# Optimization experiments

Measured on AMD Instinct MI355X. Metric: run time of the kernel, lower is better.

## Reference

```python
import jax, jax.numpy as jnp
import numpy as np

CHEBYSHEV_K = 5  # number of Chebyshev polynomial terms


def setup_inputs() -> dict:
    key = jax.random.key(0)
    k1, k2, k3 = jax.random.split(key, 3)
    B, N, F_in, F_out = 1024, 512, 16, 8
    x = jax.random.normal(k1, (B, N, F_in), dtype=jnp.float32)
    # symmetric scaled-Laplacian-like matrix, scaled small so recurrence stays stable
    A = jax.random.normal(k2, (N, N), dtype=jnp.float32) / jnp.sqrt(jnp.float32(N))
    L = 0.5 * (A + A.T)
    # xavier-uniform-like weights [K, F_in, F_out]
    limit = np.sqrt(6.0 / (F_in + F_out)).astype(np.float32)
    W = jax.random.uniform(k3, (CHEBYSHEV_K, F_in, F_out), dtype=jnp.float32,
                           minval=-limit, maxval=limit)
    b = jnp.zeros((F_out,), dtype=jnp.float32)
    return {"x": x, "L": L, "W": W, "b": b}


def reference(x, L, W, b):
    # x: [B, N, F_in], L: [N, N], W: [K, F_in, F_out], b: [F_out]
    Lx = lambda z: jnp.einsum('nm,bmf->bnf', L, z)
    Z0 = x
    Z1 = Lx(x)
    out = Z0 @ W[0] + Z1 @ W[1]
    for k in range(2, CHEBYSHEV_K):  # small fixed K, structural loop
        Zk = 2.0 * Lx(Z1) - Z0
        out = out + Zk @ W[k]
        Z0, Z1 = Z1, Zk
    return out + b
```

## Files before the change

### kernel.cpp

```cpp
#include <hip/hip_runtime.h>
#include <cstdint>
#include <cstddef>


typedef __attribute__((ext_vector_type(8))) short  frag_ab;
typedef __attribute__((ext_vector_type(4))) float  frag_cd;

constexpr int BN  = 512;
constexpr int FIN = 16;
constexpr int FOUT= 8;
constexpr int GK  = 5 * BN;
constexpr int PG  = 64;
constexpr int LDST= BN + 8;
constexpr int ZBUF= 64 * LDST;

__device__ __forceinline__ uint16_t f2bf(float f) {
    uint32_t u = __builtin_bit_cast(uint32_t, f);
    u += 0x7FFFu + ((u >> 16) & 1u);
    return (uint16_t)(u >> 16);
}
__device__ __forceinline__ float bf2f(uint16_t h) {
    uint32_t u = ((uint32_t)h) << 16;
    return __builtin_bit_cast(float, u);
}

__device__ __forceinline__ size_t pfrag(int mt, int g, int lane) {
    return ((size_t)(mt * PG + g) * 64 + lane) * 8;
}
__device__ __forceinline__ size_t pelem(int k, int row, int col) {
    return pfrag(row >> 4, (k - 1) * 16 + (col >> 5),
                 ((col >> 3) & 3) * 16 + (row & 15)) + (col & 7);
}
__device__ __forceinline__ size_t lfrag16(int mt, int kt, int lane) {
    return ((size_t)(mt * 16 + kt) * 64 + lane) * 8;
}
__device__ __forceinline__ size_t aswz(int row, int k) {
    return lfrag16(row >> 4, k >> 5, ((k >> 3) & 3) * 16 + (row & 15)) + (k & 7);
}
__device__ __forceinline__ size_t yfrag(int jt16, int g, int lane) {
    return ((size_t)(jt16 * 80 + g) * 64 + lane) * 8;
}

__global__ __launch_bounds__(256)
void prep(const float* __restrict__ x, const float* __restrict__ Lf,
          const float* __restrict__ W, uint16_t* __restrict__ Pcat,
          uint16_t* __restrict__ Llo, uint16_t* __restrict__ Yf) {
    int bid = blockIdx.x, tid = threadIdx.x;
    if (bid < 2048) {
        int t = bid * 256 + tid;
        int jlow = t & 15;
        int moct = (t >> 4) & 63;
        int jhi  = t >> 10;
        int b  = jhi * 2 + (jlow >> 3);
        int fo = jlow & 7;
        int m0 = moct * 8;
        float wr[5][16];
#pragma unroll
        for (int k = 0; k < 5; ++k)
#pragma unroll
            for (int f = 0; f < 16; ++f)
                wr[k][f] = W[(k * 16 + f) * 8 + fo];
        float tmp[5][8];
        const float* xb = x + (size_t)b * (BN * FIN) + (size_t)m0 * FIN;
#pragma unroll
        for (int r = 0; r < 8; ++r) {
            float xr[16];
#pragma unroll
            for (int fi = 0; fi < 4; ++fi) {
                float4 u = *reinterpret_cast<const float4*>(xb + r * FIN + fi * 4);
                xr[fi * 4 + 0] = u.x; xr[fi * 4 + 1] = u.y;
                xr[fi * 4 + 2] = u.z; xr[fi * 4 + 3] = u.w;
            }
#pragma unroll
            for (int k = 0; k < 5; ++k) {
                float s = 0.f;
#pragma unroll
                for (int f = 0; f < 16; ++f) s += xr[f] * wr[k][f];
                tmp[k][r] = s;
            }
        }
#pragma unroll
        for (int k = 0; k < 5; ++k) {
            frag_ab o;
#pragma unroll
            for (int j = 0; j < 8; ++j) o[j] = (short)f2bf(tmp[k][j]);
            *reinterpret_cast<frag_ab*>(
                Yf + yfrag(jhi, k * 16 + (moct >> 2), (moct & 3) * 16 + jlow)) = o;
        }
    } else {
        int t = (bid - 2048) * 256 + tid;
        int lane = t & 63, f = t >> 6;
        int mt = f >> 4, kt = f & 15;
        int row = mt * 16 + (lane & 15);
        int k0  = kt * 32 + (lane >> 4) * 8;
        const float4* p = reinterpret_cast<const float4*>(Lf + (size_t)row * BN + k0);
        float4 u0 = p[0], u1 = p[1];
        float v[8] = {u0.x, u0.y, u0.z, u0.w, u1.x, u1.y, u1.z, u1.w};
        frag_ab hi, lo;
#pragma unroll
        for (int j = 0; j < 8; ++j) {
            uint16_t h = f2bf(v[j]);
            hi[j] = (short)h;
            lo[j] = (short)f2bf(v[j] - bf2f(h));
        }
        *reinterpret_cast<frag_ab*>(Pcat + pfrag(mt, kt, lane)) = hi;
        *reinterpret_cast<frag_ab*>(Llo + lfrag16(mt, kt, lane)) = lo;
    }
}

__global__ __launch_bounds__(512)
void p2k(uint16_t* __restrict__ Pcat, const uint16_t* __restrict__ Llo,
         uint16_t* __restrict__ P2lo) {
    int tid = threadIdx.x, wv = tid >> 6, lane = tid & 63;
    int lr = lane & 15, q = lane >> 4;
    int id = blockIdx.x * 8 + wv;
    int to = id >> 5, jt = id & 31;
    frag_cd acc = {0.f, 0.f, 0.f, 0.f};
#pragma unroll
    for (int ks = 0; ks < 16; ++ks) {
        frag_ab ahi = *reinterpret_cast<const frag_ab*>(Pcat + pfrag(to, ks, lane));
        frag_ab alo = *reinterpret_cast<const frag_ab*>(Llo + lfrag16(to, ks, lane));
        frag_ab bhi = *reinterpret_cast<const frag_ab*>(Pcat + pfrag(jt, ks, lane));
        frag_ab blo = *reinterpret_cast<const frag_ab*>(Llo + lfrag16(jt, ks, lane));
        acc = __builtin_amdgcn_mfma_f32_16x16x32_bf16(ahi, bhi, acc, 0, 0, 0);
        acc = __builtin_amdgcn_mfma_f32_16x16x32_bf16(alo, bhi, acc, 0, 0, 0);
        acc = __builtin_amdgcn_mfma_f32_16x16x32_bf16(ahi, blo, acc, 0, 0, 0);
    }
#pragma unroll
    for (int r = 0; r < 4; ++r) {
        int row = to * 16 + q * 4 + r, col = jt * 16 + lr;
        float v = 2.f * acc[r] - ((row == col) ? 1.f : 0.f);
        uint16_t h = f2bf(v);
        Pcat[pelem(2, row, col)] = h;
        P2lo[aswz(row, col)] = f2bf(v - bf2f(h));
    }
}

__global__ __launch_bounds__(512)
void p34k(uint16_t* __restrict__ Pcat, const uint16_t* __restrict__ Llo,
          const uint16_t* __restrict__ P2lo) {
    int tid = threadIdx.x, wv = tid >> 6, lane = tid & 63;
    int lr = lane & 15, q = lane >> 4;
    int id = blockIdx.x * 8 + wv;
    bool isP3 = id < 1024;
    int id2 = isP3 ? id : id - 1024;
    int to = id2 >> 5, jt = id2 & 31;
    int agoff = isP3 ? 0 : 16;
    const uint16_t* aLo = isP3 ? Llo : P2lo;
    frag_cd acc = {0.f, 0.f, 0.f, 0.f};
#pragma unroll
    for (int ks = 0; ks < 16; ++ks) {
        frag_ab ahi = *reinterpret_cast<const frag_ab*>(Pcat + pfrag(to, agoff + ks, lane));
        frag_ab alo = *reinterpret_cast<const frag_ab*>(aLo + lfrag16(to, ks, lane));
        frag_ab bhi = *reinterpret_cast<const frag_ab*>(Pcat + pfrag(jt, 16 + ks, lane));
        frag_ab blo = *reinterpret_cast<const frag_ab*>(P2lo + lfrag16(jt, ks, lane));
        acc = __builtin_amdgcn_mfma_f32_16x16x32_bf16(ahi, bhi, acc, 0, 0, 0);
        acc = __builtin_amdgcn_mfma_f32_16x16x32_bf16(alo, bhi, acc, 0, 0, 0);
        acc = __builtin_amdgcn_mfma_f32_16x16x32_bf16(ahi, blo, acc, 0, 0, 0);
    }
#pragma unroll
    for (int r = 0; r < 4; ++r) {
        int row = to * 16 + q * 4 + r, col = jt * 16 + lr;
        if (isP3) {
            float sub = bf2f(Pcat[pelem(1, row, col)]) + bf2f(Llo[aswz(row, col)]);
            Pcat[pelem(3, row, col)] = f2bf(2.f * acc[r] - sub);
        } else {
            float sub = (row == col) ? 1.f : 0.f;
            Pcat[pelem(4, row, col)] = f2bf(2.f * acc[r] - sub);
        }
    }
}

__global__ __launch_bounds__(512)
void chebgemm(const uint16_t* __restrict__ Pcat, const uint16_t* __restrict__ Yf,
              const float* __restrict__ bvec, float* __restrict__ out) {
    __shared__ float fbuf[16384];
    int bid = blockIdx.x;
    int xcd = bid & 7, n = bid >> 3;
    int jt  = xcd * 8 + (n >> 2);
    int mtB = n & 3;
    int tid = threadIdx.x, wv = tid >> 6, lane = tid & 63;
    int lr = lane & 15, q = lane >> 4;
    int wm = wv >> 2, wj = wv & 3;

    frag_cd acc[4][2] = {};
#pragma unroll 2
    for (int kt = 0; kt < 64; ++kt) {
        frag_ab aF[4], bF[2];
#pragma unroll
        for (int mi = 0; mi < 4; ++mi)
            aF[mi] = *reinterpret_cast<const frag_ab*>(
                Pcat + pfrag(mtB * 8 + wm * 4 + mi, kt, lane));
#pragma unroll
        for (int cj = 0; cj < 2; ++cj)
            bF[cj] = *reinterpret_cast<const frag_ab*>(
                Yf + yfrag(jt * 8 + wj * 2 + cj, 16 + kt, lane));
#pragma unroll
        for (int mi = 0; mi < 4; ++mi)
#pragma unroll
            for (int cj = 0; cj < 2; ++cj)
                acc[mi][cj] = __builtin_amdgcn_mfma_f32_16x16x32_bf16(
                    aF[mi], bF[cj], acc[mi][cj], 0, 0, 0);
    }
#pragma unroll
    for (int mi = 0; mi < 4; ++mi)
#pragma unroll
        for (int cj = 0; cj < 2; ++cj) {
            int jt16 = jt * 8 + wj * 2 + cj;
#pragma unroll
            for (int r = 0; r < 4; ++r) {
                int nloc = wm * 64 + mi * 16 + q * 4 + r;
                int ng = mtB * 128 + nloc;
                float y0 = bf2f(Yf[yfrag(jt16, ng >> 5, ((ng >> 3) & 3) * 16 + lr)
                                   + (ng & 7)]);
                fbuf[nloc * 128 + wj * 32 + cj * 16 + lr] = acc[mi][cj][r] + y0;
            }
        }
    __syncthreads();
    float4 bv0 = *reinterpret_cast<const float4*>(bvec);
    float4 bv1 = *(reinterpret_cast<const float4*>(bvec) + 1);
#pragma unroll
    for (int i = 0; i < 8; ++i) {
        int idx = i * 2048 + tid * 4;
        int bb = idx >> 10, r = idx & 1023, nn = r >> 3, fo = r & 7;
        float4 v = *reinterpret_cast<const float4*>(fbuf + nn * 128 + bb * 8 + fo);
        float4 bias = (fo & 4) ? bv1 : bv0;
        v.x += bias.x; v.y += bias.y; v.z += bias.z; v.w += bias.w;
        *reinterpret_cast<float4*>(out + (size_t)(jt * 16 + bb) * 4096
                                       + (size_t)(mtB * 128 + nn) * 8 + fo) = v;
    }
}


__global__ __launch_bounds__(256)
void cvtL_swz(const float* __restrict__ Lf, uint16_t* __restrict__ Lb) {
    int t = blockIdx.x * 256 + threadIdx.x;
    int f = t >> 6, lane = t & 63;
    int mt = f >> 4, ks = f & 15;
    int row = mt * 16 + (lane & 15);
    int k0  = ks * 32 + (lane >> 4) * 8;
    const float4* p = reinterpret_cast<const float4*>(Lf + (size_t)row * BN + k0);
    float4 u0 = p[0], u1 = p[1];
    frag_ab o;
    o[0] = (short)f2bf(u0.x); o[1] = (short)f2bf(u0.y);
    o[2] = (short)f2bf(u0.z); o[3] = (short)f2bf(u0.w);
    o[4] = (short)f2bf(u1.x); o[5] = (short)f2bf(u1.y);
    o[6] = (short)f2bf(u1.z); o[7] = (short)f2bf(u1.w);
    *reinterpret_cast<frag_ab*>(Lb + (size_t)t * 8) = o;
}

__global__ __launch_bounds__(256)
void m2comp(const float* __restrict__ Lf, uint16_t* __restrict__ Mb) {
    const int tid = threadIdx.x;
    const int wv = tid >> 6, lane = tid & 63, lr = lane & 15, q = lane >> 4;
    const int i0 = (blockIdx.x >> 4) * 32 + (wv >> 1) * 16;
    const int j0 = (blockIdx.x & 15) * 32 + (wv & 1) * 16;
    frag_cd acc = {0.f, 0.f, 0.f, 0.f};
    const float* arow = Lf + (size_t)(i0 + lr) * BN;
    const float* brow = Lf + (size_t)(j0 + lr) * BN;
    for (int ks = 0; ks < 16; ++ks) {
        const int kb = ks * 32 + q * 8;
        const float4* ap = reinterpret_cast<const float4*>(arow + kb);
        const float4* bp = reinterpret_cast<const float4*>(brow + kb);
        float4 A0 = ap[0], A1 = ap[1], B0 = bp[0], B1 = bp[1];
        float av[8] = {A0.x, A0.y, A0.z, A0.w, A1.x, A1.y, A1.z, A1.w};
        float bw[8] = {B0.x, B0.y, B0.z, B0.w, B1.x, B1.y, B1.z, B1.w};
        frag_ab ah, al, bh, bl;
#pragma unroll
        for (int j = 0; j < 8; ++j) {
            uint16_t h = f2bf(av[j]);
            ah[j] = (short)h; al[j] = (short)f2bf(av[j] - bf2f(h));
            uint16_t g = f2bf(bw[j]);
            bh[j] = (short)g; bl[j] = (short)f2bf(bw[j] - bf2f(g));
        }
        acc = __builtin_amdgcn_mfma_f32_16x16x32_bf16(ah, bh, acc, 0, 0, 0);
        acc = __builtin_amdgcn_mfma_f32_16x16x32_bf16(ah, bl, acc, 0, 0, 0);
        acc = __builtin_amdgcn_mfma_f32_16x16x32_bf16(al, bh, acc, 0, 0, 0);
    }
#pragma unroll
    for (int r = 0; r < 4; ++r) {
        int i = i0 + q * 4 + r, j = j0 + lr;
        float v = 2.f * acc[r] - ((i == j) ? 1.f : 0.f);
        Mb[aswz(i, j)] = f2bf(v);
    }
}

__global__ __launch_bounds__(512, 2)
void cheb2_kernel(const float* __restrict__ x, const uint16_t* __restrict__ Lb,
                  const uint16_t* __restrict__ Mb, const float* __restrict__ W,
                  const float* __restrict__ bvec, float* __restrict__ out) {
    __shared__ uint16_t ldsb[2 * ZBUF];
    uint16_t* z0 = ldsb;
    uint16_t* z1 = ldsb + ZBUF;
    const int tid = threadIdx.x, wave = tid >> 6, lane = tid & 63;
    const int lr = lane & 15, q = lane >> 4;

    const float4* x4 = reinterpret_cast<const float4*>(x + (size_t)blockIdx.x * (4 * BN * FIN));
    for (int s = 0; s < 2; ++s) {
        int a = tid + s * 512;
        int f0g = a & 3, n8 = (a >> 2) & 63, bl = a >> 8;
        int jb = bl * 2048 + n8 * 32 + f0g;
        float4 v[8];
#pragma unroll
        for (int r = 0; r < 8; ++r) v[r] = x4[jb + r * 4];
        int cb = bl * 16 + f0g * 4, nb = n8 * 8;
#pragma unroll
        for (int w = 0; w < 4; ++w) {
            frag_ab pk;
#pragma unroll
            for (int r = 0; r < 8; ++r)
                pk[r] = (short)f2bf(reinterpret_cast<const float*>(&v[r])[w]);
            *reinterpret_cast<frag_ab*>(&z0[(cb + w) * LDST + nb]) = pk;
        }
    }
    frag_ab wf[3];
#pragma unroll
    for (int p = 0; p < 3; ++p) {
        frag_ab t;
#pragma unroll
        for (int jj = 0; jj < 8; ++jj) {
            int k = q * 8 + jj, ki = p * 2 + (k >> 4), fin = k & 15;
            float val = 0.0f;
            if (lr < 8) {
                int idx = fin * FOUT + lr;
                if      (ki == 0) val = W[idx] - W[4 * 128 + idx];
                else if (ki == 1) val = W[128 + idx] - W[3 * 128 + idx];
                else if (ki < 5)  val = W[ki * 128 + idx];
            }
            t[jj] = (short)f2bf(val);
        }
        wf[p] = t;
    }
    const float bv = (lr < 8) ? bvec[lr] : 0.0f;
    frag_cd accOut[4][4] = {};
    frag_cd acc1[4][4], acc2[4][4];

    auto round = [&](const uint16_t* cur) {
#pragma unroll
        for (int mi = 0; mi < 4; ++mi)
#pragma unroll
            for (int ct = 0; ct < 4; ++ct) {
                acc1[mi][ct] = (frag_cd){0.f, 0.f, 0.f, 0.f};
                acc2[mi][ct] = (frag_cd){0.f, 0.f, 0.f, 0.f};
            }
        for (int ks = 0; ks < 16; ++ks) {
            frag_ab bfr[4];
#pragma unroll
            for (int ct = 0; ct < 4; ++ct)
                bfr[ct] = *reinterpret_cast<const frag_ab*>(
                    cur + (ct * 16 + lr) * LDST + ks * 32 + q * 8);
#pragma unroll
            for (int mi = 0; mi < 4; ++mi) {
                frag_ab a = *reinterpret_cast<const frag_ab*>(
                    Lb + lfrag16(wave + mi * 8, ks, lane));
                frag_ab m = *reinterpret_cast<const frag_ab*>(
                    Mb + lfrag16(wave + mi * 8, ks, lane));
#pragma unroll
                for (int ct = 0; ct < 4; ++ct)
                    acc1[mi][ct] = __builtin_amdgcn_mfma_f32_16x16x32_bf16(
                        a, bfr[ct], acc1[mi][ct], 0, 0, 0);
#pragma unroll
                for (int ct = 0; ct < 4; ++ct)
                    acc2[mi][ct] = __builtin_amdgcn_mfma_f32_16x16x32_bf16(
                        m, bfr[ct], acc2[mi][ct], 0, 0, 0);
            }
        }
    };
    auto wb = [&](frag_cd (&acc)[4][4], uint16_t* dst, float scale) {
#pragma unroll
        for (int mi = 0; mi < 4; ++mi) {
            int row0 = (wave + mi * 8) * 16 + q * 4;
#pragma unroll
            for (int ct = 0; ct < 4; ++ct) {
                uint16_t* dp = dst + (ct * 16 + lr) * LDST + row0;
                ushort4 nv;
                nv.x = f2bf(scale * acc[mi][ct][0]); nv.y = f2bf(scale * acc[mi][ct][1]);
                nv.z = f2bf(scale * acc[mi][ct][2]); nv.w = f2bf(scale * acc[mi][ct][3]);
                *reinterpret_cast<ushort4*>(dp) = nv;
            }
        }
    };
    auto epi = [&](const uint16_t* bA, const uint16_t* bB, frag_ab wfr) {
        const uint16_t* base = (q < 2) ? bA : bB;
        int finb = (q & 1) * 8;
#pragma unroll
        for (int mi = 0; mi < 4; ++mi) {
            int n = (wave + mi * 8) * 16 + lr;
#pragma unroll
            for (int bt = 0; bt < 4; ++bt) {
                const uint16_t* pp = base + (bt * 16 + finb) * LDST + n;
                frag_ab afr;
#pragma unroll
                for (int jj = 0; jj < 8; ++jj) afr[jj] = (short)pp[jj * LDST];
                accOut[mi][bt] = __builtin_amdgcn_mfma_f32_16x16x32_bf16(
                    afr, wfr, accOut[mi][bt], 0, 0, 0);
            }
        }
    };

    __syncthreads();
    round(z0);
    wb(acc1, z1, 1.f);
    __syncthreads();
    epi(z0, z1, wf[0]);
    __syncthreads();
    wb(acc2, z0, 1.f);
    __syncthreads();
    round(z0);
    wb(acc1, z1, 2.f);
    __syncthreads();
    epi(z0, z1, wf[1]);
    __syncthreads();
    wb(acc2, z0, 2.f);
    __syncthreads();
    epi(z0, z0, wf[2]);

    float* fbuf = reinterpret_cast<float*>(z1);
    if (lr < 8) {
#pragma unroll
        for (int mi = 0; mi < 4; ++mi) {
            int n0 = (wave + mi * 8) * 16 + q * 4;
#pragma unroll
            for (int bt = 0; bt < 4; ++bt)
#pragma unroll
                for (int r = 0; r < 4; ++r)
                    fbuf[(bt * BN + n0 + r) * FOUT + lr] = accOut[mi][bt][r] + bv;
        }
    }
    __syncthreads();
    {
        const float4* fb4 = reinterpret_cast<const float4*>(fbuf);
        float4* o4 = reinterpret_cast<float4*>(out + (size_t)blockIdx.x * (4 * BN * FOUT));
#pragma unroll
        for (int i = 0; i < 8; ++i)
            o4[i * 512 + tid] = fb4[i * 512 + tid];
    }
}

__global__ __launch_bounds__(512, 2)
void cheb1_kernel(const float* __restrict__ x, const float* __restrict__ Lf,
                  const float* __restrict__ W, const float* __restrict__ bvec,
                  float* __restrict__ out) {
    __shared__ uint16_t ldsb[2 * ZBUF];
    uint16_t* z0 = ldsb;
    uint16_t* z1 = ldsb + ZBUF;
    const int tid = threadIdx.x, wave = tid >> 6, lane = tid & 63;
    const int lr = lane & 15, q = lane >> 4;
    const float4* x4 = reinterpret_cast<const float4*>(x + (size_t)blockIdx.x * (4 * BN * FIN));
    for (int s = 0; s < 2; ++s) {
        int a = tid + s * 512;
        int f0g = a & 3, n8 = (a >> 2) & 63, bl = a >> 8;
        int jb = bl * 2048 + n8 * 32 + f0g;
        float4 v[8];
#pragma unroll
        for (int r = 0; r < 8; ++r) v[r] = x4[jb + r * 4];
        int cb = bl * 16 + f0g * 4, nb = n8 * 8;
#pragma unroll
        for (int w = 0; w < 4; ++w) {
            frag_ab pk;
#pragma unroll
            for (int r = 0; r < 8; ++r)
                pk[r] = (short)f2bf(reinterpret_cast<const float*>(&v[r])[w]);
            *reinterpret_cast<frag_ab*>(&z0[(cb + w) * LDST + nb]) = pk;
        }
    }
    frag_ab wf[3];
#pragma unroll
    for (int p = 0; p < 3; ++p) {
        frag_ab t;
#pragma unroll
        for (int jj = 0; jj < 8; ++jj) {
            int k = q * 8 + jj, ki = p * 2 + (k >> 4), fin = k & 15;
            float val = (lr < 8 && ki < 5) ? W[ki * 128 + fin * FOUT + lr] : 0.0f;
            t[jj] = (short)f2bf(val);
        }
        wf[p] = t;
    }
    const float bv = (lr < 8) ? bvec[lr] : 0.0f;
    frag_cd accOut[4][4] = {};
    auto loadA = [&](int mt, int ks) -> frag_ab {
        const float4* p = reinterpret_cast<const float4*>(Lf + (size_t)(mt * 16 + lr) * BN + ks * 32 + q * 8);
        float4 u0 = p[0], u1 = p[1];
        frag_ab t;
        t[0] = (short)f2bf(u0.x); t[1] = (short)f2bf(u0.y);
        t[2] = (short)f2bf(u0.z); t[3] = (short)f2bf(u0.w);
        t[4] = (short)f2bf(u1.x); t[5] = (short)f2bf(u1.y);
        t[6] = (short)f2bf(u1.z); t[7] = (short)f2bf(u1.w);
        return t;
    };
    auto app = [&](const uint16_t* cur, uint16_t* dst, bool first) {
        frag_cd acc[4][4] = {};
        for (int ks = 0; ks < 16; ++ks) {
            frag_ab bfr[4];
#pragma unroll
            for (int ct = 0; ct < 4; ++ct)
                bfr[ct] = *reinterpret_cast<const frag_ab*>(
                    cur + (ct * 16 + lr) * LDST + ks * 32 + q * 8);
#pragma unroll
            for (int mi = 0; mi < 4; ++mi) {
                frag_ab a = loadA(wave + mi * 8, ks);
#pragma unroll
                for (int ct = 0; ct < 4; ++ct)
                    acc[mi][ct] = __builtin_amdgcn_mfma_f32_16x16x32_bf16(
                        a, bfr[ct], acc[mi][ct], 0, 0, 0);
            }
        }
#pragma unroll
        for (int mi = 0; mi < 4; ++mi) {
            int row0 = (wave + mi * 8) * 16 + q * 4;
#pragma unroll
            for (int ct = 0; ct < 4; ++ct) {
                uint16_t* dp = dst + (ct * 16 + lr) * LDST + row0;
                float pz[4] = {0.f, 0.f, 0.f, 0.f};
                if (!first) {
                    ushort4 pv = *reinterpret_cast<const ushort4*>(dp);
                    pz[0] = bf2f(pv.x); pz[1] = bf2f(pv.y);
                    pz[2] = bf2f(pv.z); pz[3] = bf2f(pv.w);
                }
                ushort4 nv;
                float v0 = acc[mi][ct][0], v1 = acc[mi][ct][1];
                float v2 = acc[mi][ct][2], v3 = acc[mi][ct][3];
                if (!first) { v0 = 2.f*v0-pz[0]; v1 = 2.f*v1-pz[1];
                              v2 = 2.f*v2-pz[2]; v3 = 2.f*v3-pz[3]; }
                nv.x = f2bf(v0); nv.y = f2bf(v1); nv.z = f2bf(v2); nv.w = f2bf(v3);
                *reinterpret_cast<ushort4*>(dp) = nv;
            }
        }
    };
    auto epi = [&](const uint16_t* bA, const uint16_t* bB, frag_ab wfr) {
        const uint16_t* base = (q < 2) ? bA : bB;
        int finb = (q & 1) * 8;
#pragma unroll
        for (int mi = 0; mi < 4; ++mi) {
            int n = (wave + mi * 8) * 16 + lr;
#pragma unroll
            for (int bt = 0; bt < 4; ++bt) {
                const uint16_t* pp = base + (bt * 16 + finb) * LDST + n;
                frag_ab afr;
#pragma unroll
                for (int jj = 0; jj < 8; ++jj) afr[jj] = (short)pp[jj * LDST];
                accOut[mi][bt] = __builtin_amdgcn_mfma_f32_16x16x32_bf16(
                    afr, wfr, accOut[mi][bt], 0, 0, 0);
            }
        }
    };
    __syncthreads();
    app(z0, z1, true);  __syncthreads();
    epi(z0, z1, wf[0]); __syncthreads();
    app(z1, z0, false); __syncthreads();
    app(z0, z1, false); __syncthreads();
    epi(z0, z1, wf[1]); __syncthreads();
    app(z1, z0, false); __syncthreads();
    epi(z0, z0, wf[2]);
    if (lr < 8) {
        float* ob = out + (size_t)blockIdx.x * 4 * BN * FOUT;
#pragma unroll
        for (int mi = 0; mi < 4; ++mi) {
            int row0 = (wave + mi * 8) * 16 + q * 4;
#pragma unroll
            for (int bt = 0; bt < 4; ++bt) {
                float* op = ob + bt * (BN * FOUT) + row0 * FOUT + lr;
                op[0] = accOut[mi][bt][0] + bv; op[FOUT] = accOut[mi][bt][1] + bv;
                op[2 * FOUT] = accOut[mi][bt][2] + bv; op[3 * FOUT] = accOut[mi][bt][3] + bv;
            }
        }
    }
}

extern "C" void kernel_launch(void* const* d_in, const int* in_sizes, int n_in,
                              void* d_out, int out_size, void* d_ws, size_t ws_size,
                              hipStream_t stream) {
    const float* x  = (const float*)d_in[0];
    const float* Lf = (const float*)d_in[1];
    const float* W  = (const float*)d_in[2];
    const float* bv = (const float*)d_in[3];
    float* out = (float*)d_out;

    const size_t PCAT_B = (size_t)32 * PG * 64 * 8 * 2;
    const size_t LLO_B  = (size_t)BN * BN * 2;
    const size_t P2LO_B = LLO_B;
    const size_t YF_B   = (size_t)512 * 80 * 64 * 8 * 2;
    const size_t matB   = (size_t)BN * BN * 2;

    if (ws_size >= PCAT_B + LLO_B + P2LO_B + YF_B) {
        uint16_t* Pcat = (uint16_t*)d_ws;
        uint16_t* Llo  = Pcat + PCAT_B / 2;
        uint16_t* P2lo = Pcat + (PCAT_B + LLO_B) / 2;
        uint16_t* Yf   = Pcat + (PCAT_B + LLO_B + P2LO_B) / 2;
        prep    <<<dim3(2176), dim3(256), 0, stream>>>(x, Lf, W, Pcat, Llo, Yf);
        p2k     <<<dim3(128),  dim3(512), 0, stream>>>(Pcat, Llo, P2lo);
        p34k    <<<dim3(256),  dim3(512), 0, stream>>>(Pcat, Llo, P2lo);
        chebgemm<<<dim3(256),  dim3(512), 0, stream>>>(Pcat, Yf, bv, out);
    } else if (ws_size >= 2 * matB) {
        uint16_t* Lb = (uint16_t*)d_ws;
        uint16_t* Mb = Lb + (size_t)BN * BN;
        cvtL_swz<<<dim3(128), dim3(256), 0, stream>>>(Lf, Lb);
        m2comp  <<<dim3(256), dim3(256), 0, stream>>>(Lf, Mb);
        cheb2_kernel<<<dim3(256), dim3(512), 0, stream>>>(x, Lb, Mb, W, bv, out);
    } else {
        cheb1_kernel<<<dim3(256), dim3(512), 0, stream>>>(x, Lf, W, bv, out);
    }
}
```

Before: 150.9 us.

## Fuse prep, P2, P3/P4 and Chebyshev GEMM into one cooperative kernel

Replaces the four-kernel sequence (prep, p2k, p34k, chebgemm) with a single cooperative megakernel that uses grid.sync() between phases, with a fallback to the old launches if the cooperative launch fails. The goal is to remove three kernel launch gaps and their tail effects. The fused kernel runs only 256 blocks of 512 threads, so the x@W precompute and Laplacian conversion phases get less parallelism than the old 2176-block prep launch. It also removes the cheb2 fallback path.

```diff
diff --git a/kernel.cpp b/kernel.cpp
--- a/kernel.cpp
+++ b/kernel.cpp
@@ -1,6 +1,9 @@
 #include <hip/hip_runtime.h>
+#include <hip/hip_cooperative_groups.h>
 #include <cstdint>
 #include <cstddef>
+
+namespace cg = cooperative_groups;
 
 
 typedef __attribute__((ext_vector_type(8))) short  frag_ab;
@@ -9,7 +12,6 @@
 constexpr int BN  = 512;
 constexpr int FIN = 16;
 constexpr int FOUT= 8;
-constexpr int GK  = 5 * BN;
 constexpr int PG  = 64;
 constexpr int LDST= BN + 8;
 constexpr int ZBUF= 64 * LDST;
@@ -40,6 +42,201 @@
 __device__ __forceinline__ size_t yfrag(int jt16, int g, int lane) {
     return ((size_t)(jt16 * 80 + g) * 64 + lane) * 8;
 }
+
+__global__ __launch_bounds__(512, 2)
+void megak(const float* __restrict__ x, const float* __restrict__ Lf,
+           const float* __restrict__ W, uint16_t* __restrict__ Pcat,
+           uint16_t* __restrict__ Llo, uint16_t* __restrict__ P2lo,
+           uint16_t* __restrict__ Yf, const float* __restrict__ bvec,
+           float* __restrict__ out) {
+    __shared__ float fbuf[16384];
+    cg::grid_group grid = cg::this_grid();
+    const int tid  = threadIdx.x;
+    const int gtid = blockIdx.x * 512 + tid;
+
+    {
+        int task = gtid >> 1, half = gtid & 1;
+        int b    = task >> 6;
+        int moct = task & 63;
+        int jhi  = b >> 1;
+        int jl0  = (b & 1) * 8;
+        const float* xb = x + (size_t)b * (BN * FIN)
+                            + (size_t)(moct * 8 + half * 4) * FIN;
+        float xr[4][16];
+#pragma unroll
+        for (int r = 0; r < 4; ++r)
+#pragma unroll
+            for (int fi = 0; fi < 4; ++fi) {
+                float4 u = *reinterpret_cast<const float4*>(xb + (size_t)r * FIN + fi * 4);
+                xr[r][fi * 4 + 0] = u.x; xr[r][fi * 4 + 1] = u.y;
+                xr[r][fi * 4 + 2] = u.z; xr[r][fi * 4 + 3] = u.w;
+            }
+#pragma unroll
+        for (int k = 0; k < 5; ++k) {
+            float a[8][4] = {};
+#pragma unroll
+            for (int f = 0; f < 16; ++f) {
+                float x0 = xr[0][f], x1 = xr[1][f], x2 = xr[2][f], x3 = xr[3][f];
+#pragma unroll
+                for (int fo = 0; fo < 8; ++fo) {
+                    float w = W[(k * 16 + f) * 8 + fo];
+                    a[fo][0] += x0 * w; a[fo][1] += x1 * w;
+                    a[fo][2] += x2 * w; a[fo][3] += x3 * w;
+                }
+            }
+#pragma unroll
+            for (int fo = 0; fo < 8; ++fo) {
+                ushort4 o;
+                o.x = f2bf(a[fo][0]); o.y = f2bf(a[fo][1]);
+                o.z = f2bf(a[fo][2]); o.w = f2bf(a[fo][3]);
+                *reinterpret_cast<ushort4*>(
+                    Yf + yfrag(jhi, k * 16 + (moct >> 2), (moct & 3) * 16 + jl0 + fo)
+                       + half * 4) = o;
+            }
+        }
+    }
+    if (gtid < 32768) {
+        int t = gtid;
+        int lane = t & 63, f = t >> 6;
+        int mt = f >> 4, kt = f & 15;
+        int row = mt * 16 + (lane & 15);
+        int k0  = kt * 32 + (lane >> 4) * 8;
+        const float4* p = reinterpret_cast<const float4*>(Lf + (size_t)row * BN + k0);
+        float4 u0 = p[0], u1 = p[1];
+        float v[8] = {u0.x, u0.y, u0.z, u0.w, u1.x, u1.y, u1.z, u1.w};
+        frag_ab hi, lo;
+#pragma unroll
+        for (int j = 0; j < 8; ++j) {
+            uint16_t h = f2bf(v[j]);
+            hi[j] = (short)h;
+            lo[j] = (short)f2bf(v[j] - bf2f(h));
+        }
+        *reinterpret_cast<frag_ab*>(Pcat + pfrag(mt, kt, lane)) = hi;
+        *reinterpret_cast<frag_ab*>(Llo + lfrag16(mt, kt, lane)) = lo;
+    }
+    grid.sync();
+
+    {
+        int wv = tid >> 6, lane = tid & 63;
+        int lr = lane & 15, q = lane >> 4;
+        if (blockIdx.x < 128) {
+            int id = blockIdx.x * 8 + wv;
+            int to = id >> 5, jt = id & 31;
+            frag_cd acc = {0.f, 0.f, 0.f, 0.f};
+#pragma unroll
+            for (int ks = 0; ks < 16; ++ks) {
+                frag_ab ahi = *reinterpret_cast<const frag_ab*>(Pcat + pfrag(to, ks, lane));
+                frag_ab alo = *reinterpret_cast<const frag_ab*>(Llo + lfrag16(to, ks, lane));
+                frag_ab bhi = *reinterpret_cast<const frag_ab*>(Pcat + pfrag(jt, ks, lane));
+                frag_ab blo = *reinterpret_cast<const frag_ab*>(Llo + lfrag16(jt, ks, lane));
+                acc = __builtin_amdgcn_mfma_f32_16x16x32_bf16(ahi, bhi, acc, 0, 0, 0);
+                acc = __builtin_amdgcn_mfma_f32_16x16x32_bf16(alo, bhi, acc, 0, 0, 0);
+                acc = __builtin_amdgcn_mfma_f32_16x16x32_bf16(ahi, blo, acc, 0, 0, 0);
+            }
+#pragma unroll
+            for (int r = 0; r < 4; ++r) {
+                int row = to * 16 + q * 4 + r, col = jt * 16 + lr;
+                float v = 2.f * acc[r] - ((row == col) ? 1.f : 0.f);
+                uint16_t h = f2bf(v);
+                Pcat[pelem(2, row, col)] = h;
+                P2lo[aswz(row, col)] = f2bf(v - bf2f(h));
+            }
+        }
+    }
+    grid.sync();
+
+    {
+        int wv = tid >> 6, lane = tid & 63;
+        int lr = lane & 15, q = lane >> 4;
+        int id = blockIdx.x * 8 + wv;
+        bool isP3 = id < 1024;
+        int id2 = isP3 ? id : id - 1024;
+        int to = id2 >> 5, jt = id2 & 31;
+        int agoff = isP3 ? 0 : 16;
+        const uint16_t* aLo = isP3 ? Llo : P2lo;
+        frag_cd acc = {0.f, 0.f, 0.f, 0.f};
+#pragma unroll
+        for (int ks = 0; ks < 16; ++ks) {
+            frag_ab ahi = *reinterpret_cast<const frag_ab*>(Pcat + pfrag(to, agoff + ks, lane));
+            frag_ab alo = *reinterpret_cast<const frag_ab*>(aLo + lfrag16(to, ks, lane));
+            frag_ab bhi = *reinterpret_cast<const frag_ab*>(Pcat + pfrag(jt, 16 + ks, lane));
+            frag_ab blo = *reinterpret_cast<const frag_ab*>(P2lo + lfrag16(jt, ks, lane));
+            acc = __builtin_amdgcn_mfma_f32_16x16x32_bf16(ahi, bhi, acc, 0, 0, 0);
+            acc = __builtin_amdgcn_mfma_f32_16x16x32_bf16(alo, bhi, acc, 0, 0, 0);
+            acc = __builtin_amdgcn_mfma_f32_16x16x32_bf16(ahi, blo, acc, 0, 0, 0);
+        }
+#pragma unroll
+        for (int r = 0; r < 4; ++r) {
+            int row = to * 16 + q * 4 + r, col = jt * 16 + lr;
+            if (isP3) {
+                float sub = bf2f(Pcat[pelem(1, row, col)]) + bf2f(Llo[aswz(row, col)]);
+                Pcat[pelem(3, row, col)] = f2bf(2.f * acc[r] - sub);
+            } else {
+                float sub = (row == col) ? 1.f : 0.f;
+                Pcat[pelem(4, row, col)] = f2bf(2.f * acc[r] - sub);
+            }
+        }
+    }
+    grid.sync();
+
+    {
+        int bid = blockIdx.x;
+        int xcd = bid & 7, n = bid >> 3;
+        int jt  = xcd * 8 + (n >> 2);
+        int mtB = n & 3;
+        int wv = tid >> 6, lane = tid & 63;
+        int lr = lane & 15, q = lane >> 4;
+        int wm = wv >> 2, wj = wv & 3;
+
+        frag_cd acc[4][2] = {};
+#pragma unroll 2
+        for (int kt = 0; kt < 64; ++kt) {
+            frag_ab aF[4], bF[2];
+#pragma unroll
+            for (int mi = 0; mi < 4; ++mi)
+                aF[mi] = *reinterpret_cast<const frag_ab*>(
+                    Pcat + pfrag(mtB * 8 + wm * 4 + mi, kt, lane));
+#pragma unroll
+            for (int cj = 0; cj < 2; ++cj)
+                bF[cj] = *reinterpret_cast<const frag_ab*>(
+                    Yf + yfrag(jt * 8 + wj * 2 + cj, 16 + kt, lane));
+#pragma unroll
+            for (int mi = 0; mi < 4; ++mi)
+#pragma unroll
+                for (int cj = 0; cj < 2; ++cj)
+                    acc[mi][cj] = __builtin_amdgcn_mfma_f32_16x16x32_bf16(
+                        aF[mi], bF[cj], acc[mi][cj], 0, 0, 0);
+        }
+#pragma unroll
+        for (int mi = 0; mi < 4; ++mi)
+#pragma unroll
+            for (int cj = 0; cj < 2; ++cj) {
+                int jt16 = jt * 8 + wj * 2 + cj;
+#pragma unroll
+                for (int r = 0; r < 4; ++r) {
+                    int nloc = wm * 64 + mi * 16 + q * 4 + r;
+                    int ng = mtB * 128 + nloc;
+                    float y0 = bf2f(Yf[yfrag(jt16, ng >> 5, ((ng >> 3) & 3) * 16 + lr)
+                                       + (ng & 7)]);
+                    fbuf[nloc * 128 + wj * 32 + cj * 16 + lr] = acc[mi][cj][r] + y0;
+                }
+            }
+        __syncthreads();
+        float4 bv0 = *reinterpret_cast<const float4*>(bvec);
+        float4 bv1 = *(reinterpret_cast<const float4*>(bvec) + 1);
+#pragma unroll
+        for (int i = 0; i < 8; ++i) {
+            int idx = i * 2048 + tid * 4;
+            int bb = idx >> 10, r = idx & 1023, nn = r >> 3, fo = r & 7;
+            float4 v = *reinterpret_cast<const float4*>(fbuf + nn * 128 + bb * 8 + fo);
+            float4 bias = (fo & 4) ? bv1 : bv0;
+            v.x += bias.x; v.y += bias.y; v.z += bias.z; v.w += bias.w;
+            *reinterpret_cast<float4*>(out + (size_t)(jt * 16 + bb) * 4096
+                                           + (size_t)(mtB * 128 + nn) * 8 + fo) = v;
+        }
+    }
+}
+
 
 __global__ __launch_bounds__(256)
 void prep(const float* __restrict__ x, const float* __restrict__ Lf,
@@ -228,212 +425,6 @@
         v.x += bias.x; v.y += bias.y; v.z += bias.z; v.w += bias.w;
         *reinterpret_cast<float4*>(out + (size_t)(jt * 16 + bb) * 4096
                                        + (size_t)(mtB * 128 + nn) * 8 + fo) = v;
-    }
-}
-
-
-__global__ __launch_bounds__(256)
-void cvtL_swz(const float* __restrict__ Lf, uint16_t* __restrict__ Lb) {
-    int t = blockIdx.x * 256 + threadIdx.x;
-    int f = t >> 6, lane = t & 63;
-    int mt = f >> 4, ks = f & 15;
-    int row = mt * 16 + (lane & 15);
-    int k0  = ks * 32 + (lane >> 4) * 8;
-    const float4* p = reinterpret_cast<const float4*>(Lf + (size_t)row * BN + k0);
-    float4 u0 = p[0], u1 = p[1];
-    frag_ab o;
-    o[0] = (short)f2bf(u0.x); o[1] = (short)f2bf(u0.y);
-    o[2] = (short)f2bf(u0.z); o[3] = (short)f2bf(u0.w);
-    o[4] = (short)f2bf(u1.x); o[5] = (short)f2bf(u1.y);
-    o[6] = (short)f2bf(u1.z); o[7] = (short)f2bf(u1.w);
-    *reinterpret_cast<frag_ab*>(Lb + (size_t)t * 8) = o;
-}
-
-__global__ __launch_bounds__(256)
-void m2comp(const float* __restrict__ Lf, uint16_t* __restrict__ Mb) {
-    const int tid = threadIdx.x;
-    const int wv = tid >> 6, lane = tid & 63, lr = lane & 15, q = lane >> 4;
-    const int i0 = (blockIdx.x >> 4) * 32 + (wv >> 1) * 16;
-    const int j0 = (blockIdx.x & 15) * 32 + (wv & 1) * 16;
-    frag_cd acc = {0.f, 0.f, 0.f, 0.f};
-    const float* arow = Lf + (size_t)(i0 + lr) * BN;
-    const float* brow = Lf + (size_t)(j0 + lr) * BN;
-    for (int ks = 0; ks < 16; ++ks) {
-        const int kb = ks * 32 + q * 8;
-        const float4* ap = reinterpret_cast<const float4*>(arow + kb);
-        const float4* bp = reinterpret_cast<const float4*>(brow + kb);
-        float4 A0 = ap[0], A1 = ap[1], B0 = bp[0], B1 = bp[1];
-        float av[8] = {A0.x, A0.y, A0.z, A0.w, A1.x, A1.y, A1.z, A1.w};
-        float bw[8] = {B0.x, B0.y, B0.z, B0.w, B1.x, B1.y, B1.z, B1.w};
-        frag_ab ah, al, bh, bl;
-#pragma unroll
-        for (int j = 0; j < 8; ++j) {
-            uint16_t h = f2bf(av[j]);
-            ah[j] = (short)h; al[j] = (short)f2bf(av[j] - bf2f(h));
-            uint16_t g = f2bf(bw[j]);
-            bh[j] = (short)g; bl[j] = (short)f2bf(bw[j] - bf2f(g));
-        }
-        acc = __builtin_amdgcn_mfma_f32_16x16x32_bf16(ah, bh, acc, 0, 0, 0);
-        acc = __builtin_amdgcn_mfma_f32_16x16x32_bf16(ah, bl, acc, 0, 0, 0);
-        acc = __builtin_amdgcn_mfma_f32_16x16x32_bf16(al, bh, acc, 0, 0, 0);
-    }
-#pragma unroll
-    for (int r = 0; r < 4; ++r) {
-        int i = i0 + q * 4 + r, j = j0 + lr;
-        float v = 2.f * acc[r] - ((i == j) ? 1.f : 0.f);
-        Mb[aswz(i, j)] = f2bf(v);
-    }
-}
-
-__global__ __launch_bounds__(512, 2)
-void cheb2_kernel(const float* __restrict__ x, const uint16_t* __restrict__ Lb,
-                  const uint16_t* __restrict__ Mb, const float* __restrict__ W,
-                  const float* __restrict__ bvec, float* __restrict__ out) {
-    __shared__ uint16_t ldsb[2 * ZBUF];
-    uint16_t* z0 = ldsb;
-    uint16_t* z1 = ldsb + ZBUF;
-    const int tid = threadIdx.x, wave = tid >> 6, lane = tid & 63;
-    const int lr = lane & 15, q = lane >> 4;
-
-    const float4* x4 = reinterpret_cast<const float4*>(x + (size_t)blockIdx.x * (4 * BN * FIN));
-    for (int s = 0; s < 2; ++s) {
-        int a = tid + s * 512;
-        int f0g = a & 3, n8 = (a >> 2) & 63, bl = a >> 8;
-        int jb = bl * 2048 + n8 * 32 + f0g;
-        float4 v[8];
-#pragma unroll
-        for (int r = 0; r < 8; ++r) v[r] = x4[jb + r * 4];
-        int cb = bl * 16 + f0g * 4, nb = n8 * 8;
-#pragma unroll
-        for (int w = 0; w < 4; ++w) {
-            frag_ab pk;
-#pragma unroll
-            for (int r = 0; r < 8; ++r)
-                pk[r] = (short)f2bf(reinterpret_cast<const float*>(&v[r])[w]);
-            *reinterpret_cast<frag_ab*>(&z0[(cb + w) * LDST + nb]) = pk;
-        }
-    }
-    frag_ab wf[3];
-#pragma unroll
-    for (int p = 0; p < 3; ++p) {
-        frag_ab t;
-#pragma unroll
-        for (int jj = 0; jj < 8; ++jj) {
-            int k = q * 8 + jj, ki = p * 2 + (k >> 4), fin = k & 15;
-            float val = 0.0f;
-            if (lr < 8) {
-                int idx = fin * FOUT + lr;
-                if      (ki == 0) val = W[idx] - W[4 * 128 + idx];
-                else if (ki == 1) val = W[128 + idx] - W[3 * 128 + idx];
-                else if (ki < 5)  val = W[ki * 128 + idx];
-            }
-            t[jj] = (short)f2bf(val);
-        }
-        wf[p] = t;
-    }
-    const float bv = (lr < 8) ? bvec[lr] : 0.0f;
-    frag_cd accOut[4][4] = {};
-    frag_cd acc1[4][4], acc2[4][4];
-
-    auto round = [&](const uint16_t* cur) {
-#pragma unroll
-        for (int mi = 0; mi < 4; ++mi)
-#pragma unroll
-            for (int ct = 0; ct < 4; ++ct) {
-                acc1[mi][ct] = (frag_cd){0.f, 0.f, 0.f, 0.f};
-                acc2[mi][ct] = (frag_cd){0.f, 0.f, 0.f, 0.f};
-            }
-        for (int ks = 0; ks < 16; ++ks) {
-            frag_ab bfr[4];
-#pragma unroll
-            for (int ct = 0; ct < 4; ++ct)
-                bfr[ct] = *reinterpret_cast<const frag_ab*>(
-                    cur + (ct * 16 + lr) * LDST + ks * 32 + q * 8);
-#pragma unroll
-            for (int mi = 0; mi < 4; ++mi) {
-                frag_ab a = *reinterpret_cast<const frag_ab*>(
-                    Lb + lfrag16(wave + mi * 8, ks, lane));
-                frag_ab m = *reinterpret_cast<const frag_ab*>(
-                    Mb + lfrag16(wave + mi * 8, ks, lane));
-#pragma unroll
-                for (int ct = 0; ct < 4; ++ct)
-                    acc1[mi][ct] = __builtin_amdgcn_mfma_f32_16x16x32_bf16(
-                        a, bfr[ct], acc1[mi][ct], 0, 0, 0);
-#pragma unroll
-                for (int ct = 0; ct < 4; ++ct)
-                    acc2[mi][ct] = __builtin_amdgcn_mfma_f32_16x16x32_bf16(
-                        m, bfr[ct], acc2[mi][ct], 0, 0, 0);
-            }
-        }
-    };
-    auto wb = [&](frag_cd (&acc)[4][4], uint16_t* dst, float scale) {
-#pragma unroll
-        for (int mi = 0; mi < 4; ++mi) {
-            int row0 = (wave + mi * 8) * 16 + q * 4;
-#pragma unroll
-            for (int ct = 0; ct < 4; ++ct) {
-                uint16_t* dp = dst + (ct * 16 + lr) * LDST + row0;
-                ushort4 nv;
-                nv.x = f2bf(scale * acc[mi][ct][0]); nv.y = f2bf(scale * acc[mi][ct][1]);
-                nv.z = f2bf(scale * acc[mi][ct][2]); nv.w = f2bf(scale * acc[mi][ct][3]);
-                *reinterpret_cast<ushort4*>(dp) = nv;
-            }
-        }
-    };
-    auto epi = [&](const uint16_t* bA, const uint16_t* bB, frag_ab wfr) {
-        const uint16_t* base = (q < 2) ? bA : bB;
-        int finb = (q & 1) * 8;
-#pragma unroll
-        for (int mi = 0; mi < 4; ++mi) {
-            int n = (wave + mi * 8) * 16 + lr;
-#pragma unroll
-            for (int bt = 0; bt < 4; ++bt) {
-                const uint16_t* pp = base + (bt * 16 + finb) * LDST + n;
-                frag_ab afr;
-#pragma unroll
-                for (int jj = 0; jj < 8; ++jj) afr[jj] = (short)pp[jj * LDST];
-                accOut[mi][bt] = __builtin_amdgcn_mfma_f32_16x16x32_bf16(
-                    afr, wfr, accOut[mi][bt], 0, 0, 0);
-            }
-        }
-    };
-
-    __syncthreads();
-    round(z0);
-    wb(acc1, z1, 1.f);
-    __syncthreads();
-    epi(z0, z1, wf[0]);
-    __syncthreads();
-    wb(acc2, z0, 1.f);
-    __syncthreads();
-    round(z0);
-    wb(acc1, z1, 2.f);
-    __syncthreads();
-    epi(z0, z1, wf[1]);
-    __syncthreads();
-    wb(acc2, z0, 2.f);
-    __syncthreads();
-    epi(z0, z0, wf[2]);
-
-    float* fbuf = reinterpret_cast<float*>(z1);
-    if (lr < 8) {
-#pragma unroll
-        for (int mi = 0; mi < 4; ++mi) {
-            int n0 = (wave + mi * 8) * 16 + q * 4;
-#pragma unroll
-            for (int bt = 0; bt < 4; ++bt)
-#pragma unroll
-                for (int r = 0; r < 4; ++r)
-                    fbuf[(bt * BN + n0 + r) * FOUT + lr] = accOut[mi][bt][r] + bv;
-        }
-    }
-    __syncthreads();
-    {
-        const float4* fb4 = reinterpret_cast<const float4*>(fbuf);
-        float4* o4 = reinterpret_cast<float4*>(out + (size_t)blockIdx.x * (4 * BN * FOUT));
-#pragma unroll
-        for (int i = 0; i < 8; ++i)
-            o4[i * 512 + tid] = fb4[i * 512 + tid];
     }
 }
 
@@ -580,23 +571,25 @@
     const size_t LLO_B  = (size_t)BN * BN * 2;
     const size_t P2LO_B = LLO_B;
     const size_t YF_B   = (size_t)512 * 80 * 64 * 8 * 2;
-    const size_t matB   = (size_t)BN * BN * 2;
 
     if (ws_size >= PCAT_B + LLO_B + P2LO_B + YF_B) {
         uint16_t* Pcat = (uint16_t*)d_ws;
         uint16_t* Llo  = Pcat + PCAT_B / 2;
         uint16_t* P2lo = Pcat + (PCAT_B + LLO_B) / 2;
         uint16_t* Yf   = Pcat + (PCAT_B + LLO_B + P2LO_B) / 2;
-        prep    <<<dim3(2176), dim3(256), 0, stream>>>(x, Lf, W, Pcat, Llo, Yf);
-        p2k     <<<dim3(128),  dim3(512), 0, stream>>>(Pcat, Llo, P2lo);
-        p34k    <<<dim3(256),  dim3(512), 0, stream>>>(Pcat, Llo, P2lo);
-        chebgemm<<<dim3(256),  dim3(512), 0, stream>>>(Pcat, Yf, bv, out);
-    } else if (ws_size >= 2 * matB) {
-        uint16_t* Lb = (uint16_t*)d_ws;
-        uint16_t* Mb = Lb + (size_t)BN * BN;
-        cvtL_swz<<<dim3(128), dim3(256), 0, stream>>>(Lf, Lb);
-        m2comp  <<<dim3(256), dim3(256), 0, stream>>>(Lf, Mb);
-        cheb2_kernel<<<dim3(256), dim3(512), 0, stream>>>(x, Lb, Mb, W, bv, out);
+
+        void* kargs[] = {(void*)&x, (void*)&Lf, (void*)&W, (void*)&Pcat,
+                         (void*)&Llo, (void*)&P2lo, (void*)&Yf, (void*)&bv,
+                         (void*)&out};
+        hipError_t ce = hipLaunchCooperativeKernel(
+            (const void*)megak, dim3(256), dim3(512), kargs, 0, stream);
+        if (ce != hipSuccess) {
+            (void)hipGetLastError();
+            prep    <<<dim3(2176), dim3(256), 0, stream>>>(x, Lf, W, Pcat, Llo, Yf);
+            p2k     <<<dim3(128),  dim3(512), 0, stream>>>(Pcat, Llo, P2lo);
+            p34k    <<<dim3(256),  dim3(512), 0, stream>>>(Pcat, Llo, P2lo);
+            chebgemm<<<dim3(256),  dim3(512), 0, stream>>>(Pcat, Yf, bv, out);
+        }
     } else {
         cheb1_kernel<<<dim3(256), dim3(512), 0, stream>>>(x, Lf, W, bv, out);
     }
```

Result: slower. 270.8 us (+79.4%).
